# Kernel optimization log

Hardware: AMD Instinct MI355X
Metric: run time of the kernel (lower is better)

## Reference

```python
import jax, jax.numpy as jnp
import numpy as np

TOP_K = 8
EPS_NORM = 1e-12  # torch F.normalize eps
EPS_ENT = 1e-9

B, N, D = 8, 1024, 512


def setup_inputs() -> dict:
    key = jax.random.key(0)
    ks = jax.random.split(key, 16)
    inp = {}
    for i in range(8):
        inp[f"band{i}"] = jax.random.normal(ks[i], (B, N, D), dtype=jnp.float32)
    s = 1.0 / np.sqrt(D)
    inp["qW"] = jax.random.normal(ks[8], (8, D, D), dtype=jnp.float32) * s
    inp["qb"] = jax.random.normal(ks[9], (8, D), dtype=jnp.float32) * s
    inp["kW"] = jax.random.normal(ks[10], (8, D, D), dtype=jnp.float32) * s
    inp["kb"] = jax.random.normal(ks[11], (8, D), dtype=jnp.float32) * s
    inp["vW"] = jax.random.normal(ks[12], (8, D, D), dtype=jnp.float32) * s
    inp["vb"] = jax.random.normal(ks[13], (8, D), dtype=jnp.float32) * s
    return inp


def _l2norm(x):
    n = jnp.linalg.norm(x, axis=-1, keepdims=True)
    return x / jnp.maximum(n, EPS_NORM)


def _cross_attend(q_band, kv_band, q_idx, k_idx, qW, qb, kW, kb, vW, vb):
    # Linear: x @ W.T + b
    Q = jnp.einsum('bnd,ed->bne', q_band, qW[q_idx]) + qb[q_idx]
    K = jnp.einsum('bnd,ed->bne', kv_band, kW[k_idx]) + kb[k_idx]
    V = jnp.einsum('bnd,ed->bne', kv_band, vW[k_idx]) + vb[k_idx]
    Qn, Kn = _l2norm(Q), _l2norm(K)
    scores = jnp.einsum('bqd,bkd->bqk', Qn, Kn)  # cosine sims, [B,Nq,Nk]
    b, nq, nk = scores.shape
    _, idx = jax.lax.top_k(scores, TOP_K)  # [B,Nq,k]
    mask = jnp.zeros(scores.shape, dtype=bool).at[
        jnp.arange(b)[:, None, None], jnp.arange(nq)[None, :, None], idx
    ].set(True)
    scores = jnp.where(mask, scores, -jnp.inf)
    attn = jax.nn.softmax(scores, axis=-1)
    entropy = -(attn * jnp.log(attn + EPS_ENT)).sum(-1).mean(1)  # [B]
    out = jnp.einsum('bqk,bkd->bqd', attn, V)
    return out, entropy


def reference(band0, band1, band2, band3, band4, band5, band6, band7,
              qW, qb, kW, kb, vW, vb):
    bands = [band0, band1, band2, band3, band4, band5, band6, band7]
    outputs = list(bands)
    entropies = []

    def ca(qi, ki):
        return _cross_attend(bands[qi], bands[ki], qi, ki, qW, qb, kW, kb, vW, vb)

    # complementary pairs
    for lo, hi in [(0, 6), (1, 5), (2, 4)]:
        o, e = ca(hi, lo)
        outputs[hi] = outputs[hi] + o
        entropies.append(e)
        o, e = ca(lo, hi)
        outputs[lo] = outputs[lo] + o
        entropies.append(e)
    # bridge band 3 -> all spectral
    for i in [0, 1, 2, 4, 5, 6]:
        o, e = ca(i, 3)
        outputs[i] = outputs[i] + 0.5 * o
        entropies.append(e)
    # temporal band 7 -> all
    for i in range(7):
        o, e = ca(i, 7)
        outputs[i] = outputs[i] + 0.5 * o
        entropies.append(e)

    return jnp.stack(outputs, 0), jnp.stack(entropies, 0)  # [8,B,N,D], [19,B]
```

## Files before the change

### kernel.cpp

```cpp
#include <hip/hip_runtime.h>
#include <math.h>

#define B_ 8
#define N_ 1024
#define D_ 512
#define BAND_ELEMS (B_ * N_ * D_)
#define OUT_MAIN (8L * BAND_ELEMS)
#define NCALLS 19

struct Ptrs8 { const float* p[8]; };
struct CallTab { int qi[NCALLS]; int ki[NCALLS]; };
struct MergeTab { int ncalls[8]; int calls[8][3]; int kis[NCALLS]; float wts[NCALLS]; };

typedef __attribute__((ext_vector_type(8))) short bf16x8;
typedef __attribute__((ext_vector_type(4))) float f32x4;

__device__ __forceinline__ ushort f2bf_rne(float x) {
  uint u = __float_as_uint(x);
  return (ushort)((u + 0x7fffu + ((u >> 16) & 1u)) >> 16);
}

#define GLOAD16(gsrc, ldst)                                                   \
  __builtin_amdgcn_global_load_lds(                                          \
      (const __attribute__((address_space(1))) void*)(gsrc),                 \
      (__attribute__((address_space(3))) void*)(ldst), 16, 0, 0)
#define GLOAD4(gsrc, ldst)                                                    \
  __builtin_amdgcn_global_load_lds(                                          \
      (const __attribute__((address_space(1))) void*)(gsrc),                 \
      (__attribute__((address_space(3))) void*)(ldst), 4, 0, 0)

#define BM 128
#define BN 128
#define BK 16
#define LDP 132

__device__ __forceinline__ int bgran(int g) {
  return (g & ~7) | ((g + (g >> 3)) & 7);
}

__device__ __forceinline__ void gemm_core(const float* __restrict__ A,
                                          const float* __restrict__ Bm,
                                          int m0, int n0, int K,
                                          float (&acc)[8][8]) {
  __shared__ float As[BK * LDP];
  __shared__ float Bs[BK * LDP];

  const int t = threadIdx.x;
  const int tx = t & 15, ty = t >> 4;
  const int rs = t >> 2;
  const int cs = t & 3;

  float4 pa[2], pb[2];
#pragma unroll
  for (int it = 0; it < 2; ++it) {
    pa[it] = *(const float4*)(A + (long)(m0 + rs + 64 * it) * K + cs * 4);
    pb[it] = *(const float4*)(Bm + (long)(n0 + rs + 64 * it) * K + cs * 4);
  }

  for (int k0 = 0; k0 < K; k0 += BK) {
    __syncthreads();
    {
      const int sa = ((cs & 1) << 2);
      const int base = cs * 4 * LDP;
#pragma unroll
      for (int it = 0; it < 2; ++it) {
        const int r = rs + 64 * it;
        const int ra = r ^ sa;
        As[base + 0 * LDP + ra] = pa[it].x;
        As[base + 1 * LDP + ra] = pa[it].y;
        As[base + 2 * LDP + ra] = pa[it].z;
        As[base + 3 * LDP + ra] = pa[it].w;
        const int rb = bgran(r >> 2) * 4 + (r & 3);
        Bs[base + 0 * LDP + rb] = pb[it].x;
        Bs[base + 1 * LDP + rb] = pb[it].y;
        Bs[base + 2 * LDP + rb] = pb[it].z;
        Bs[base + 3 * LDP + rb] = pb[it].w;
      }
    }
    __syncthreads();

    if (k0 + BK < K) {
#pragma unroll
      for (int it = 0; it < 2; ++it) {
        pa[it] = *(const float4*)(A + (long)(m0 + rs + 64 * it) * K + k0 + BK + cs * 4);
        pb[it] = *(const float4*)(Bm + (long)(n0 + rs + 64 * it) * K + k0 + BK + cs * 4);
      }
    }

#pragma unroll
    for (int kk = 0; kk < BK; ++kk) {
      const int c1 = (kk >> 2) & 1;
      float a[8], b[8];
      {
        float4 u = *(const float4*)&As[kk * LDP + ty * 8 + c1 * 4];
        float4 v = *(const float4*)&As[kk * LDP + ty * 8 + 4 - c1 * 4];
        a[0] = u.x; a[1] = u.y; a[2] = u.z; a[3] = u.w;
        a[4] = v.x; a[5] = v.y; a[6] = v.z; a[7] = v.w;
        float4 p = *(const float4*)&Bs[kk * LDP + bgran(2 * tx) * 4];
        float4 q = *(const float4*)&Bs[kk * LDP + bgran(2 * tx + 1) * 4];
        b[0] = p.x; b[1] = p.y; b[2] = p.z; b[3] = p.w;
        b[4] = q.x; b[5] = q.y; b[6] = q.z; b[7] = q.w;
      }
#pragma unroll
      for (int i = 0; i < 8; ++i)
#pragma unroll
        for (int j = 0; j < 8; ++j) acc[i][j] = fmaf(a[i], b[j], acc[i][j]);
    }
  }
}

__device__ __forceinline__ void proj_epilogue(float* __restrict__ dst,
                                              const float* __restrict__ bvec,
                                              int m0, int n0, float (&acc)[8][8]) {
  const int t = threadIdx.x;
  const int tx = t & 15, ty = t >> 4;
#pragma unroll
  for (int i = 0; i < 8; ++i) {
    float* crow = dst + (long)(m0 + ty * 8 + i) * D_ + n0 + tx * 8;
    const float* bp = bvec + n0 + tx * 8;
    float4 r0, r1;
    r0.x = acc[i][0] + bp[0]; r0.y = acc[i][1] + bp[1];
    r0.z = acc[i][2] + bp[2]; r0.w = acc[i][3] + bp[3];
    r1.x = acc[i][4] + bp[4]; r1.y = acc[i][5] + bp[5];
    r1.z = acc[i][6] + bp[6]; r1.w = acc[i][7] + bp[7];
    ((float4*)crow)[0] = r0;
    ((float4*)crow)[1] = r1;
  }
}

__global__ __launch_bounds__(256) void gemm_proj_qk(Ptrs8 bands,
                                                    const float* __restrict__ qW,
                                                    const float* __restrict__ kW,
                                                    const float* __restrict__ qb,
                                                    const float* __restrict__ kb,
                                                    float* __restrict__ Qn,
                                                    float* __restrict__ Kn) {
  const int mat = blockIdx.z >> 3, band = blockIdx.z & 7;
  const float* W = (mat == 0) ? qW : kW;
  const float* bvec = (mat == 0) ? qb : kb;
  float* dst = ((mat == 0) ? Qn : Kn) + (long)band * BAND_ELEMS;
  W += (long)band * D_ * D_;
  bvec += band * D_;

  const int m0 = blockIdx.y * BM, n0 = blockIdx.x * BN;
  float acc[8][8] = {};
  gemm_core(bands.p[band], W, m0, n0, D_, acc);
  proj_epilogue(dst, bvec, m0, n0, acc);
}

__global__ __launch_bounds__(256) void gemm_proj_v(Ptrs8 bands,
                                                   const float* __restrict__ vW,
                                                   const float* __restrict__ vb,
                                                   float* __restrict__ V) {
  const int band = blockIdx.z;
  const float* W = vW + (long)band * D_ * D_;
  const float* bvec = vb + band * D_;
  float* dst = V + (long)band * BAND_ELEMS;

  const int m0 = blockIdx.y * BM, n0 = blockIdx.x * BN;
  float acc[8][8] = {};
  gemm_core(bands.p[band], W, m0, n0, D_, acc);
  proj_epilogue(dst, bvec, m0, n0, acc);
}

__global__ __launch_bounds__(256) void l2norm_rows(float* __restrict__ X,
                                                   ushort* __restrict__ bf) {
  const long row = (long)blockIdx.x * 4 + (threadIdx.x >> 6);
  const int lane = threadIdx.x & 63;
  float* p = X + row * D_;
  float4 a = ((float4*)p)[lane];
  float4 b = ((float4*)p)[lane + 64];
  float s = a.x * a.x + a.y * a.y + a.z * a.z + a.w * a.w +
            b.x * b.x + b.y * b.y + b.z * b.z + b.w * b.w;
#pragma unroll
  for (int m = 1; m < 64; m <<= 1) s += __shfl_xor(s, m);
  const float inv = 1.0f / fmaxf(sqrtf(s), 1e-12f);
  a.x *= inv; a.y *= inv; a.z *= inv; a.w *= inv;
  b.x *= inv; b.y *= inv; b.z *= inv; b.w *= inv;
  ((float4*)p)[lane] = a;
  ((float4*)p)[lane + 64] = b;
  ushort4 w0, w1;
  w0.x = f2bf_rne(a.x); w0.y = f2bf_rne(a.y); w0.z = f2bf_rne(a.z); w0.w = f2bf_rne(a.w);
  w1.x = f2bf_rne(b.x); w1.y = f2bf_rne(b.y); w1.z = f2bf_rne(b.z); w1.w = f2bf_rne(b.w);
  *(ushort4*)(bf + row * D_ + lane * 4) = w0;
  *(ushort4*)(bf + row * D_ + 256 + lane * 4) = w1;
}

#define SBM 128
#define SBN 128

__device__ __forceinline__ int gidx(int row, int oct) {
  return row * 4 + (oct ^ ((row >> 1) & 3));
}

__global__ __launch_bounds__(256) void mfma_extract_bf(const ushort* __restrict__ Qbf,
                                                       const ushort* __restrict__ Kbf,
                                                       float* __restrict__ candv,
                                                       ushort* __restrict__ candi,
                                                       CallTab tab) {
  __shared__ ushort ldsA[3][4096];
  __shared__ ushort ldsB[3][4096];

  const int z = blockIdx.z;
  const int c = z >> 3, b = z & 7;
  const ushort* A = Qbf + (long)tab.qi[c] * BAND_ELEMS + (long)b * N_ * D_;
  const ushort* Bm = Kbf + (long)tab.ki[c] * BAND_ELEMS + (long)b * N_ * D_;
  const int m0 = blockIdx.y * SBM, n0 = blockIdx.x * SBN;

  const int t = threadIdx.x;
  const int lane = t & 63;
  const int wm = t >> 6;
  const int fr = lane & 15, fh = lane >> 4;

  f32x4 acc[2][8] = {};

  const int srow_off = lane >> 2;
  const int soct = lane & 3;

#define XSTAGE(pA, pB, k0)                                                    \
  do {                                                                        \
    _Pragma("unroll")                                                         \
    for (int it_ = 0; it_ < 2; ++it_) {                                       \
      const int row0_ = wm * 32 + it_ * 16;                                   \
      const int row_ = row0_ + srow_off;                                      \
      const int oct_ = soct ^ ((row_ >> 1) & 3);                              \
      GLOAD16(A + (long)(m0 + row_) * D_ + (k0) + oct_ * 8,                   \
              (pA) + row0_ * 32);                                             \
      GLOAD16(Bm + (long)(n0 + row_) * D_ + (k0) + oct_ * 8,                  \
              (pB) + row0_ * 32);                                             \
    }                                                                         \
  } while (0)

  ushort* pA0 = &ldsA[0][0]; ushort* pB0 = &ldsB[0][0];
  ushort* pA1 = &ldsA[1][0]; ushort* pB1 = &ldsB[1][0];
  ushort* pA2 = &ldsA[2][0]; ushort* pB2 = &ldsB[2][0];

  XSTAGE(pA0, pB0, 0);
  XSTAGE(pA1, pB1, 32);

  for (int kq = 0; kq < 16; ++kq) {
    if (kq + 2 < 16) {
      XSTAGE(pA2, pB2, (kq + 2) * 32);
      asm volatile("s_waitcnt vmcnt(8)" ::: "memory");
    } else if (kq + 1 < 16) {
      asm volatile("s_waitcnt vmcnt(4)" ::: "memory");
    } else {
      asm volatile("s_waitcnt vmcnt(0)" ::: "memory");
    }
    __builtin_amdgcn_sched_barrier(0);
    __builtin_amdgcn_s_barrier();
    __builtin_amdgcn_sched_barrier(0);

    bf16x8 af[2], bfr[8];
#pragma unroll
    for (int i = 0; i < 2; ++i) {
      const int row = wm * 32 + i * 16 + fr;
      af[i] = *(const bf16x8*)&pA0[gidx(row, fh) * 8];
    }
#pragma unroll
    for (int j = 0; j < 8; ++j) {
      const int row = j * 16 + fr;
      bfr[j] = *(const bf16x8*)&pB0[gidx(row, fh) * 8];
    }

#pragma unroll
    for (int i = 0; i < 2; ++i)
#pragma unroll
      for (int j = 0; j < 8; ++j)
        acc[i][j] = __builtin_amdgcn_mfma_f32_16x16x32_bf16(af[i], bfr[j], acc[i][j], 0, 0, 0);

    __builtin_amdgcn_sched_barrier(0);
    __builtin_amdgcn_s_barrier();
    __builtin_amdgcn_sched_barrier(0);

    ushort* ta = pA0; pA0 = pA1; pA1 = pA2; pA2 = ta;
    ushort* tb = pB0; pB0 = pB1; pB1 = pB2; pB2 = tb;
  }
#undef XSTAGE

#pragma unroll
  for (int i = 0; i < 2; ++i)
#pragma unroll
    for (int rr = 0; rr < 4; ++rr) {
      const int R = b * N_ + m0 + wm * 32 + i * 16 + fh * 4 + rr;
      const long base = (((long)c * 8192 + R) * 8 + blockIdx.x) * 8;
#pragma unroll
      for (int it = 0; it < 8; ++it) {
        float lv = acc[i][0][rr]; int lj = 0;
#pragma unroll
        for (int j = 1; j < 8; ++j)
          if (acc[i][j][rr] > lv) { lv = acc[i][j][rr]; lj = j; }
        int li = lj * 16 + fr;
#pragma unroll
        for (int m = 1; m < 16; m <<= 1) {
          float ov = __shfl_xor(lv, m);
          int oi = __shfl_xor(li, m);
          if (ov > lv || (ov == lv && oi < li)) { lv = ov; li = oi; }
        }
        if (fr == it) { candv[base + it] = lv; candi[base + it] = (ushort)(n0 + li); }
        if (fr == (li & 15)) {
#pragma unroll
          for (int j = 0; j < 8; ++j)
            if (j == (li >> 4)) acc[i][j][rr] = -INFINITY;
        }
      }
    }
}

#define RRBLOCKS (NCALLS * 8192 / 4)

__global__ __launch_bounds__(256) void rerank_exact(const float* __restrict__ Qn,
                                                    const float* __restrict__ Kn,
                                                    const float* __restrict__ candv,
                                                    const ushort* __restrict__ candi,
                                                    float* __restrict__ fp,
                                                    int* __restrict__ fi,
                                                    float* __restrict__ out,
                                                    CallTab tab) {
  __shared__ float sbuf[4][2][1088];

  const int bid = blockIdx.x;
  const int blk = (bid & 7) * (RRBLOCKS / 8) + (bid >> 3);

  const int w = threadIdx.x >> 6, lane = threadIdx.x & 63;
  const long gr = (long)blk * 4 + w;
  const int c = (int)(gr >> 13);
  const int R = (int)(gr & 8191);
  const int b = R >> 10;

  const long cb = gr * 64;
  float cv = candv[cb + lane];
  int ci = (int)candi[cb + lane];

  int myi = 0;
#pragma unroll
  for (int it = 0; it < 16; ++it) {
    float lv = cv; int gi = ci;
#pragma unroll
    for (int m = 1; m < 64; m <<= 1) {
      float ov = __shfl_xor(lv, m);
      int oi = __shfl_xor(gi, m);
      if (ov > lv || (ov == lv && oi < gi)) { lv = ov; gi = oi; }
    }
    if ((lane & 15) == it) myi = gi;
    if (ci == gi) cv = -INFINITY;
  }

  const int mycand = lane & 15;
  const int eidx = __shfl(myi, mycand);

  const float* qrow = Qn + (long)tab.qi[c] * BAND_ELEMS + (long)R * D_;
  const float* ksrc0 = Kn + (long)tab.ki[c] * BAND_ELEMS +
                       ((long)(b << 10) + eidx) * D_ + ((lane >> 4) << 2);

#define STAGE(bb, ch)                                                         \
  do {                                                                        \
    float* base_ = &sbuf[w][bb][0];                                           \
    GLOAD16(ksrc0 + (ch) * 64 + 0,  base_ + 0);                               \
    GLOAD16(ksrc0 + (ch) * 64 + 16, base_ + 256);                             \
    GLOAD16(ksrc0 + (ch) * 64 + 32, base_ + 512);                             \
    GLOAD16(ksrc0 + (ch) * 64 + 48, base_ + 768);                             \
    GLOAD4(qrow + (ch) * 64 + lane, base_ + 1024);                            \
  } while (0)

  float acc = 0.f;
  STAGE(0, 0);
#pragma unroll
  for (int ch = 0; ch < 8; ++ch) {
    if (ch < 7) {
      STAGE((ch + 1) & 1, ch + 1);
      asm volatile("s_waitcnt vmcnt(5)" ::: "memory");
    } else {
      asm volatile("s_waitcnt vmcnt(0)" ::: "memory");
    }
    const float* kb2 = &sbuf[w][ch & 1][0];
    const float* qb2 = &sbuf[w][ch & 1][1024];
#pragma unroll
    for (int kq = 0; kq < 16; ++kq) {
      float4 kv = *(const float4*)(kb2 + kq * 64 + mycand * 4);
      float4 qv = *(const float4*)(qb2 + kq * 4);
      acc = fmaf(qv.x, kv.x, acc);
      acc = fmaf(qv.y, kv.y, acc);
      acc = fmaf(qv.z, kv.z, acc);
      acc = fmaf(qv.w, kv.w, acc);
    }
  }
#undef STAGE

  float ev = acc; int ei = eidx;
  float sv[8]; int si[8];
#pragma unroll
  for (int it = 0; it < 8; ++it) {
    float lv = ev; int gi = ei;
#pragma unroll
    for (int m = 1; m < 64; m <<= 1) {
      float ov = __shfl_xor(lv, m);
      int oi = __shfl_xor(gi, m);
      if (ov > lv || (ov == lv && oi < gi)) { lv = ov; gi = oi; }
    }
    sv[it] = lv; si[it] = gi;
    if (ei == gi) ev = -INFINITY;
  }

  float p[8], sum = 0.f;
#pragma unroll
  for (int j = 0; j < 8; ++j) { p[j] = expf(sv[j] - sv[0]); sum += p[j]; }
  const float isum = 1.0f / sum;
  float H = 0.f;
#pragma unroll
  for (int j = 0; j < 8; ++j) { p[j] *= isum; H -= p[j] * logf(p[j] + 1e-9f); }

  if (lane == 0) {
    atomicAdd(out + OUT_MAIN + (long)c * B_ + b, H * (1.0f / (float)N_));
#pragma unroll
    for (int j = 0; j < 8; ++j) { fp[gr * 8 + j] = p[j]; fi[gr * 8 + j] = si[j]; }
  }
}

__global__ __launch_bounds__(256) void merge_pv(Ptrs8 bands,
                                                const float* __restrict__ fp,
                                                const int* __restrict__ fi,
                                                const float* __restrict__ V,
                                                float* __restrict__ out,
                                                MergeTab mt) {
  const int bb = blockIdx.y;
  const int w = threadIdx.x >> 6, lane = threadIdx.x & 63;
  const long R = (long)blockIdx.x * 4 + w;
  const int b = (int)(R >> 10);

  float4 o0 = {0, 0, 0, 0}, o1 = {0, 0, 0, 0};
  const int nc = mt.ncalls[bb];
  for (int s = 0; s < nc; ++s) {
    const int c = mt.calls[bb][s];
    const float wt = mt.wts[c];
    const int ki = mt.kis[c];
    const long fb = ((long)c * 8192 + R) * 8;
    float4 p0 = *(const float4*)(fp + fb);
    float4 p1 = *(const float4*)(fp + fb + 4);
    int4 i0 = *(const int4*)(fi + fb);
    int4 i1 = *(const int4*)(fi + fb + 4);
    float pj[8] = {p0.x, p0.y, p0.z, p0.w, p1.x, p1.y, p1.z, p1.w};
    int ij[8] = {i0.x, i0.y, i0.z, i0.w, i1.x, i1.y, i1.z, i1.w};
#pragma unroll
    for (int j = 0; j < 8; ++j) {
      const float pw = pj[j] * wt;
      const float4* vr = (const float4*)(V + (long)ki * BAND_ELEMS +
                                         ((long)(b << 10) + ij[j]) * D_);
      float4 x0 = vr[lane * 2], x1 = vr[lane * 2 + 1];
      o0.x += pw * x0.x; o0.y += pw * x0.y; o0.z += pw * x0.z; o0.w += pw * x0.w;
      o1.x += pw * x1.x; o1.y += pw * x1.y; o1.z += pw * x1.z; o1.w += pw * x1.w;
    }
  }

  const float4* src = (const float4*)(bands.p[bb] + R * D_);
  float4 s0 = src[lane * 2], s1 = src[lane * 2 + 1];
  s0.x += o0.x; s0.y += o0.y; s0.z += o0.z; s0.w += o0.w;
  s1.x += o1.x; s1.y += o1.y; s1.z += o1.z; s1.w += o1.w;
  float4* dst = (float4*)(out + (long)bb * BAND_ELEMS + R * D_);
  dst[lane * 2] = s0;
  dst[lane * 2 + 1] = s1;
}

__global__ void init_eps(float* __restrict__ out) {
  if (threadIdx.x < NCALLS * B_) out[OUT_MAIN + threadIdx.x] = 0.f;
}

extern "C" void kernel_launch(void* const* d_in, const int* in_sizes, int n_in,
                              void* d_out, int out_size, void* d_ws, size_t ws_size,
                              hipStream_t stream) {
  Ptrs8 bands;
  for (int i = 0; i < 8; ++i) bands.p[i] = (const float*)d_in[i];
  const float* qW = (const float*)d_in[8];
  const float* qb = (const float*)d_in[9];
  const float* kW = (const float*)d_in[10];
  const float* kb = (const float*)d_in[11];
  const float* vW = (const float*)d_in[12];
  const float* vb = (const float*)d_in[13];
  float* out = (float*)d_out;
  float* ws = (float*)d_ws;

  float* Qn = ws;
  float* Kn = ws + (long)8 * BAND_ELEMS;
  float* V = ws + (long)16 * BAND_ELEMS;
  ushort* bfbuf = (ushort*)V;
  float* candv = ws + (long)24 * BAND_ELEMS;
  ushort* candi = (ushort*)(candv + (long)NCALLS * 8192 * 64);
  float* fp = (float*)(candi + (long)NCALLS * 8192 * 64);
  int* fi = (int*)(fp + (long)NCALLS * 8192 * 8);

  static const int calls[NCALLS][2] = {
      {6, 0}, {0, 6}, {5, 1}, {1, 5}, {4, 2}, {2, 4},
      {0, 3}, {1, 3}, {2, 3}, {4, 3}, {5, 3}, {6, 3},
      {0, 7}, {1, 7}, {2, 7}, {3, 7}, {4, 7}, {5, 7}, {6, 7}};

  CallTab tab;
  MergeTab mt;
  for (int i = 0; i < 8; ++i) mt.ncalls[i] = 0;
  for (int c = 0; c < NCALLS; ++c) {
    tab.qi[c] = calls[c][0];
    tab.ki[c] = calls[c][1];
    mt.kis[c] = calls[c][1];
    mt.wts[c] = (c < 6) ? 1.0f : 0.5f;
    int q = calls[c][0];
    mt.calls[q][mt.ncalls[q]++] = c;
  }

  hipLaunchKernelGGL(init_eps, dim3(1), dim3(256), 0, stream, out);

  dim3 gqk(D_ / BN, (B_ * N_) / BM, 16);
  hipLaunchKernelGGL(gemm_proj_qk, gqk, dim3(256), 0, stream,
                     bands, qW, kW, qb, kb, Qn, Kn);

  hipLaunchKernelGGL(l2norm_rows, dim3(2 * 8 * B_ * N_ / 4), dim3(256), 0, stream,
                     Qn, bfbuf);

  dim3 gs(N_ / SBN, N_ / SBM, NCALLS * 8);
  hipLaunchKernelGGL(mfma_extract_bf, gs, dim3(256), 0, stream,
                     bfbuf, bfbuf + (long)8 * BAND_ELEMS, candv, candi, tab);

  dim3 gv(D_ / BN, (B_ * N_) / BM, 8);
  hipLaunchKernelGGL(gemm_proj_v, gv, dim3(256), 0, stream, bands, vW, vb, V);

  hipLaunchKernelGGL(rerank_exact, dim3(RRBLOCKS), dim3(256), 0, stream,
                     Qn, Kn, candv, candi, fp, fi, out, tab);

  hipLaunchKernelGGL(merge_pv, dim3(B_ * N_ / 4, 8), dim3(256), 0, stream,
                     bands, fp, fi, V, out, mt);
}
```

Baseline: 3.450 ms.

## Use split-bf16 MFMA for V projection and deepen extract pipeline to four stages

Replaces the fp32 SIMT GEMM for the V projection with a bf16 MFMA kernel. It splits each fp32 operand into high and low bf16 parts and accumulates three MFMA products to keep near-fp32 accuracy. Separately, the candidate-extraction MFMA kernel moves from a 3-buffer to a 4-buffer LDS ring with precomputed source and LDS offsets and a fully unrolled k loop. This removes the pointer rotation and allows one more stage of loads in flight. The split-bf16 approach drops the lo*lo term, so V differs slightly from fp32, and the larger LDS footprint may lower occupancy.

```diff
diff --git a/kernel.cpp b/kernel.cpp
--- a/kernel.cpp
+++ b/kernel.cpp
@@ -13,11 +13,15 @@
 struct MergeTab { int ncalls[8]; int calls[8][3]; int kis[NCALLS]; float wts[NCALLS]; };
 
 typedef __attribute__((ext_vector_type(8))) short bf16x8;
+typedef __attribute__((ext_vector_type(8))) ushort ushort8;
 typedef __attribute__((ext_vector_type(4))) float f32x4;
 
 __device__ __forceinline__ ushort f2bf_rne(float x) {
   uint u = __float_as_uint(x);
   return (ushort)((u + 0x7fffu + ((u >> 16) & 1u)) >> 16);
+}
+__device__ __forceinline__ float bf2f(ushort h) {
+  return __uint_as_float(((uint)h) << 16);
 }
 
 #define GLOAD16(gsrc, ldst)                                                   \
@@ -148,19 +152,102 @@
   proj_epilogue(dst, bvec, m0, n0, acc);
 }
 
-__global__ __launch_bounds__(256) void gemm_proj_v(Ptrs8 bands,
-                                                   const float* __restrict__ vW,
-                                                   const float* __restrict__ vb,
-                                                   float* __restrict__ V) {
+__global__ __launch_bounds__(256) void gemm_proj_v_mfma(Ptrs8 bands,
+                                                        const float* __restrict__ vW,
+                                                        const float* __restrict__ vb,
+                                                        float* __restrict__ V) {
+  __shared__ ushort plds[4 * 4096];
+
   const int band = blockIdx.z;
-  const float* W = vW + (long)band * D_ * D_;
+  const uint* Au = (const uint*)bands.p[band];
+  const uint* Bu = (const uint*)(vW + (long)band * D_ * D_);
   const float* bvec = vb + band * D_;
   float* dst = V + (long)band * BAND_ELEMS;
 
+  const int t = threadIdx.x;
+  const int lane = t & 63;
+  const int wave = t >> 6;
+  const int wm = wave >> 1, wn = wave & 1;
+  const int fr = lane & 15, fh = lane >> 4;
   const int m0 = blockIdx.y * BM, n0 = blockIdx.x * BN;
-  float acc[8][8] = {};
-  gemm_core(bands.p[band], W, m0, n0, D_, acc);
-  proj_epilogue(dst, bvec, m0, n0, acc);
+
+  f32x4 acc[4][4] = {};
+
+  const int sg_r[2] = {t >> 2, (t + 256) >> 2};
+  const int sg_h = t & 3;
+
+  for (int k0 = 0; k0 < D_; k0 += 32) {
+    uint4 ga[2][2], gb[2][2];
+#pragma unroll
+    for (int it = 0; it < 2; ++it) {
+      long offA = (long)(m0 + sg_r[it]) * D_ + k0 + sg_h * 8;
+      ga[it][0] = *(const uint4*)(Au + offA);
+      ga[it][1] = *(const uint4*)(Au + offA + 4);
+      long offB = (long)(n0 + sg_r[it]) * D_ + k0 + sg_h * 8;
+      gb[it][0] = *(const uint4*)(Bu + offB);
+      gb[it][1] = *(const uint4*)(Bu + offB + 4);
+    }
+    __syncthreads();
+#pragma unroll
+    for (int op = 0; op < 2; ++op) {
+#pragma unroll
+      for (int it = 0; it < 2; ++it) {
+        uint w[8];
+        {
+          uint4 w0 = op ? gb[it][0] : ga[it][0];
+          uint4 w1 = op ? gb[it][1] : ga[it][1];
+          w[0] = w0.x; w[1] = w0.y; w[2] = w0.z; w[3] = w0.w;
+          w[4] = w1.x; w[5] = w1.y; w[6] = w1.z; w[7] = w1.w;
+        }
+        ushort8 vhi, vlo;
+#pragma unroll
+        for (int e = 0; e < 8; ++e) {
+          float x = __uint_as_float(w[e]);
+          ushort hb = f2bf_rne(x);
+          ushort lb = f2bf_rne(x - bf2f(hb));
+          vhi[e] = hb;
+          vlo[e] = lb;
+        }
+        const int ds2 = (sg_h * 128 + sg_r[it]) * 8;
+        *(ushort8*)&plds[op * 4096 + ds2] = vhi;
+        *(ushort8*)&plds[(2 + op) * 4096 + ds2] = vlo;
+      }
+    }
+    __syncthreads();
+
+    bf16x8 ah[4], bh[4], al[4], bl[4];
+#pragma unroll
+    for (int i = 0; i < 4; ++i) {
+      const int ra = wm * 64 + i * 16 + fr;
+      const int rb = wn * 64 + i * 16 + fr;
+      ah[i] = *(const bf16x8*)&plds[0 * 4096 + (fh * 128 + ra) * 8];
+      bh[i] = *(const bf16x8*)&plds[1 * 4096 + (fh * 128 + rb) * 8];
+      al[i] = *(const bf16x8*)&plds[2 * 4096 + (fh * 128 + ra) * 8];
+      bl[i] = *(const bf16x8*)&plds[3 * 4096 + (fh * 128 + rb) * 8];
+    }
+
+#pragma unroll
+    for (int i = 0; i < 4; ++i)
+#pragma unroll
+      for (int j = 0; j < 4; ++j) {
+        acc[i][j] = __builtin_amdgcn_mfma_f32_16x16x32_bf16(ah[i], bh[j], acc[i][j], 0, 0, 0);
+        acc[i][j] = __builtin_amdgcn_mfma_f32_16x16x32_bf16(ah[i], bl[j], acc[i][j], 0, 0, 0);
+        acc[i][j] = __builtin_amdgcn_mfma_f32_16x16x32_bf16(al[i], bh[j], acc[i][j], 0, 0, 0);
+      }
+  }
+
+#pragma unroll
+  for (int i = 0; i < 4; ++i)
+#pragma unroll
+    for (int j = 0; j < 4; ++j) {
+      const int col = n0 + wn * 64 + j * 16 + fr;
+      const float bv = bvec[col];
+#pragma unroll
+      for (int r = 0; r < 4; ++r) {
+        const int row = m0 + wm * 64 + i * 16 + fh * 4 + r;
+        dst[(long)row * D_ + col] = acc[i][j][r] + bv;
+      }
+    }
 }
 
 __global__ __launch_bounds__(256) void l2norm_rows(float* __restrict__ X,
@@ -198,8 +285,7 @@
                                                        float* __restrict__ candv,
                                                        ushort* __restrict__ candi,
                                                        CallTab tab) {
-  __shared__ ushort ldsA[3][4096];
-  __shared__ ushort ldsB[3][4096];
+  __shared__ ushort lds[4][2][4096];
 
   const int z = blockIdx.z;
   const int c = z >> 3, b = z & 7;
@@ -214,67 +300,78 @@
 
   f32x4 acc[2][8] = {};
 
-  const int srow_off = lane >> 2;
+  const int srow = lane >> 2;
   const int soct = lane & 3;
-
-#define XSTAGE(pA, pB, k0)                                                    \
+  const ushort* sA[2];
+  const ushort* sB[2];
+  int dof[2];
+#pragma unroll
+  for (int it = 0; it < 2; ++it) {
+    const int row0 = wm * 32 + it * 16;
+    const int row = row0 + srow;
+    const int oct = soct ^ ((row >> 1) & 3);
+    sA[it] = A + (long)(m0 + row) * D_ + oct * 8;
+    sB[it] = Bm + (long)(n0 + row) * D_ + oct * 8;
+    dof[it] = row0 * 32;
+  }
+
+  int gofA[2], gofB[8];
+#pragma unroll
+  for (int i = 0; i < 2; ++i) gofA[i] = gidx(wm * 32 + i * 16 + fr, fh) * 8;
+#pragma unroll
+  for (int j = 0; j < 8; ++j) gofB[j] = gidx(j * 16 + fr, fh) * 8;
+
+  ushort* lb = &lds[0][0][0];
+
+#define XSTAGE(buf, m)                                                        \
   do {                                                                        \
-    _Pragma("unroll")                                                         \
-    for (int it_ = 0; it_ < 2; ++it_) {                                       \
-      const int row0_ = wm * 32 + it_ * 16;                                   \
-      const int row_ = row0_ + srow_off;                                      \
-      const int oct_ = soct ^ ((row_ >> 1) & 3);                              \
-      GLOAD16(A + (long)(m0 + row_) * D_ + (k0) + oct_ * 8,                   \
-              (pA) + row0_ * 32);                                             \
-      GLOAD16(Bm + (long)(n0 + row_) * D_ + (k0) + oct_ * 8,                  \
-              (pB) + row0_ * 32);                                             \
-    }                                                                         \
+    GLOAD16(sA[0] + (m) * 32, lb + ((buf) * 2 + 0) * 4096 + dof[0]);          \
+    GLOAD16(sB[0] + (m) * 32, lb + ((buf) * 2 + 1) * 4096 + dof[0]);          \
+    GLOAD16(sA[1] + (m) * 32, lb + ((buf) * 2 + 0) * 4096 + dof[1]);          \
+    GLOAD16(sB[1] + (m) * 32, lb + ((buf) * 2 + 1) * 4096 + dof[1]);          \
   } while (0)
 
-  ushort* pA0 = &ldsA[0][0]; ushort* pB0 = &ldsB[0][0];
-  ushort* pA1 = &ldsA[1][0]; ushort* pB1 = &ldsB[1][0];
-  ushort* pA2 = &ldsA[2][0]; ushort* pB2 = &ldsB[2][0];
-
-  XSTAGE(pA0, pB0, 0);
-  XSTAGE(pA1, pB1, 32);
-
-  for (int kq = 0; kq < 16; ++kq) {
-    if (kq + 2 < 16) {
-      XSTAGE(pA2, pB2, (kq + 2) * 32);
-      asm volatile("s_waitcnt vmcnt(8)" ::: "memory");
-    } else if (kq + 1 < 16) {
-      asm volatile("s_waitcnt vmcnt(4)" ::: "memory");
-    } else {
-      asm volatile("s_waitcnt vmcnt(0)" ::: "memory");
-    }
-    __builtin_amdgcn_sched_barrier(0);
-    __builtin_amdgcn_s_barrier();
-    __builtin_amdgcn_sched_barrier(0);
-
-    bf16x8 af[2], bfr[8];
-#pragma unroll
-    for (int i = 0; i < 2; ++i) {
-      const int row = wm * 32 + i * 16 + fr;
-      af[i] = *(const bf16x8*)&pA0[gidx(row, fh) * 8];
-    }
-#pragma unroll
-    for (int j = 0; j < 8; ++j) {
-      const int row = j * 16 + fr;
-      bfr[j] = *(const bf16x8*)&pB0[gidx(row, fh) * 8];
-    }
-
-#pragma unroll
-    for (int i = 0; i < 2; ++i)
+  XSTAGE(0, 0);
+  XSTAGE(1, 1);
+  XSTAGE(2, 2);
+
+#pragma unroll
+  for (int ot = 0; ot < 4; ++ot) {
+#pragma unroll
+    for (int ph = 0; ph < 4; ++ph) {
+      const int kq = ot * 4 + ph;
+      if (kq < 13) {
+        XSTAGE((ph + 3) & 3, kq + 3);
+        asm volatile("s_waitcnt vmcnt(12)" ::: "memory");
+      } else if (kq == 13) {
+        asm volatile("s_waitcnt vmcnt(8)" ::: "memory");
+      } else if (kq == 14) {
+        asm volatile("s_waitcnt vmcnt(4)" ::: "memory");
+      } else {
+        asm volatile("s_waitcnt vmcnt(0)" ::: "memory");
+      }
+      __builtin_amdgcn_sched_barrier(0);
+      __builtin_amdgcn_s_barrier();
+      __builtin_amdgcn_sched_barrier(0);
+
+      bf16x8 af[2], bfr[8];
+#pragma unroll
+      for (int i = 0; i < 2; ++i)
+        af[i] = *(const bf16x8*)(lb + (ph * 2 + 0) * 4096 + gofA[i]);
 #pragma unroll
       for (int j = 0; j < 8; ++j)
-        acc[i][j] = __builtin_amdgcn_mfma_f32_16x16x32_bf16(af[i], bfr[j], acc[i][j], 0, 0, 0);
-
-    __builtin_amdgcn_sched_barrier(0);
-    __builtin_amdgcn_s_barrier();
-    __builtin_amdgcn_sched_barrier(0);
-
-    ushort* ta = pA0; pA0 = pA1; pA1 = pA2; pA2 = ta;
-    ushort* tb = pB0; pB0 = pB1; pB1 = pB2; pB2 = tb;
+        bfr[j] = *(const bf16x8*)(lb + (ph * 2 + 1) * 4096 + gofB[j]);
+
+#pragma unroll
+      for (int i = 0; i < 2; ++i)
+#pragma unroll
+        for (int j = 0; j < 8; ++j)
+          acc[i][j] = __builtin_amdgcn_mfma_f32_16x16x32_bf16(af[i], bfr[j], acc[i][j], 0, 0, 0);
+
+      __builtin_amdgcn_sched_barrier(0);
+      __builtin_amdgcn_s_barrier();
+      __builtin_amdgcn_sched_barrier(0);
+    }
   }
 #undef XSTAGE
 
@@ -519,7 +616,7 @@
                      bfbuf, bfbuf + (long)8 * BAND_ELEMS, candv, candi, tab);
 
   dim3 gv(D_ / BN, (B_ * N_) / BM, 8);
-  hipLaunchKernelGGL(gemm_proj_v, gv, dim3(256), 0, stream, bands, vW, vb, V);
+  hipLaunchKernelGGL(gemm_proj_v_mfma, gv, dim3(256), 0, stream, bands, vW, vb, V);
 
   hipLaunchKernelGGL(rerank_exact, dim3(RRBLOCKS), dim3(256), 0, stream,
                      Qn, Kn, candv, candi, fp, fi, out, tab);
```

After: 3.100 ms. -10.1%, faster.
